# Optimization experiments

Hardware: AMD Instinct MI355X
Metric: run time of the kernel (lower is better)

The kernel has to match this reference:

```python
import jax, jax.numpy as jnp
import numpy as np

D_MODEL = 256
D_INNER = 512
D_STATE = 16
DT_RANK = 16
D_CONV = 4


def _layernorm(x, g, b):
    m = x.mean(-1, keepdims=True)
    v = jnp.mean((x - m) ** 2, axis=-1, keepdims=True)
    return (x - m) * jax.lax.rsqrt(v + 1e-5) * g + b


def _mamba(x, p):
    # x: (B, L, D); faithful to mamba_ssm Mamba forward (selective_scan_ref)
    in_w, conv_w, conv_b, xp_w, dt_w, dt_b, A_log, Dp, out_w = p
    B, L, _ = x.shape
    xz = x @ in_w.T                                   # (B, L, 2*d_inner)
    xi, z = jnp.split(xz, 2, axis=-1)
    # causal depthwise conv over time (d_conv=4), truncated to L
    xpad = jnp.pad(xi, ((0, 0), (D_CONV - 1, 0), (0, 0)))
    xc = conv_b + sum(xpad[:, k:k + L, :] * conv_w[:, k] for k in range(D_CONV))
    xc = jax.nn.silu(xc)                              # u: (B, L, d_inner)
    dbl = xc @ xp_w.T                                 # (B, L, dt_rank + 2*d_state)
    dt = dbl[..., :DT_RANK]
    Bm = dbl[..., DT_RANK:DT_RANK + D_STATE]          # (B, L, n)
    Cm = dbl[..., DT_RANK + D_STATE:]                 # (B, L, n)
    delta = jax.nn.softplus(dt @ dt_w.T + dt_b)       # (B, L, d_inner)
    A = -jnp.exp(A_log)                               # (d_inner, n)
    dA = jnp.exp(jnp.einsum('bld,dn->bldn', delta, A))
    dBu = jnp.einsum('bld,bln,bld->bldn', delta, Bm, xc)

    def step(h, inp):
        dA_t, dBu_t, C_t = inp
        h = dA_t * h + dBu_t                          # (B, d_inner, n)
        return h, jnp.einsum('bdn,bn->bd', h, C_t)

    h0 = jnp.zeros((B, D_INNER, D_STATE), x.dtype)
    _, ys = jax.lax.scan(step, h0, (dA.transpose(1, 0, 2, 3),
                                    dBu.transpose(1, 0, 2, 3),
                                    Cm.transpose(1, 0, 2)))
    y = ys.transpose(1, 0, 2) + xc * Dp               # (B, L, d_inner)
    y = y * jax.nn.silu(z)
    return y @ out_w.T                                # (B, L, D)


def _encoder(layer_params, x):
    # layer_params leaves have leading axis = num_layers (3)
    def step(carry, p):
        h = _layernorm(carry, p[0], p[1])
        return h + _mamba(h, p[2:]), None
    out, _ = jax.lax.scan(step, x, layer_params)
    return out


def _forward(x1, x2, x3, x4, audio, vis_w, vis_b, ln_g, ln_b, in_w, conv_w,
             conv_b, xp_w, dt_w, dt_b, A_log, Dp, out_w, gate_w, gate_b):
    gamma = 1.0
    bt = x1.shape[0]
    B = bt // 10
    d = x1.shape[1]
    pooled = [x.mean((2, 3)).reshape(B, 10, d) for x in (x1, x2, x3, x4)]
    vis = [p @ vis_w[i].T + vis_b[i] for i, p in enumerate(pooled)]
    # encoders 0..3: audio, 4..7: video scales
    stacked = jnp.stack([audio, audio, audio, audio] + vis)     # (8, B, 10, d)
    enc_params = (ln_g, ln_b, in_w, conv_w, conv_b, xp_w, dt_w, dt_b, A_log, Dp, out_w)
    outs = jax.vmap(_encoder)(enc_params, stacked)              # (8, B, 10, d)
    gates = jax.nn.silu(jnp.einsum('ebld,eod->eblo', outs, gate_w)
                        + gate_b[:, None, None, :])
    # NOTE: gate1 is reshaped WITHOUT transpose (faithful to original code)
    ag1 = gates[0].reshape(bt, d, 1, 1)
    ag2 = jnp.transpose(gates[1], (1, 0, 2)).reshape(bt, d, 1, 1)
    ag3 = jnp.transpose(gates[2], (1, 0, 2)).reshape(bt, d, 1, 1)
    ag4 = jnp.transpose(gates[3], (1, 0, 2)).reshape(bt, d, 1, 1)
    vg = sum(jnp.transpose(gates[4 + i], (1, 0, 2)).reshape(bt, d)
             for i in range(4)) / 4.0
    x1o = x1 + ag1 * x1 * gamma
    x2o = x2 + ag2 * x2 * gamma
    x3o = x3 + ag3 * x3 * gamma
    x4o = x4 + ag4 * x4 * gamma
    af = audio.reshape(bt, d)
    ao = (af + vg * af * gamma)[:, :, None]                     # (bt, d, 1)
    return (x4o, x3o, x2o, x1o, ao)


def setup_inputs() -> dict:
    key = jax.random.key(0)
    ks = jax.random.split(key, 24)
    s = 0.05
    n = lambda k, shp: jax.random.normal(k, shp, dtype=jnp.float32)
    inp = {
        'x1': n(ks[0], (40, 256, 56, 56)),
        'x2': n(ks[1], (40, 256, 28, 28)),
        'x3': n(ks[2], (40, 256, 14, 14)),
        'x4': n(ks[3], (40, 256, 7, 7)),
        'audio': n(ks[4], (4, 10, 256)),
        'vis_w': n(ks[5], (4, 256, 256)) * s,
        'vis_b': n(ks[6], (4, 256)) * s,
        'ln_g': jnp.ones((8, 3, 256), jnp.float32),
        'ln_b': jnp.zeros((8, 3, 256), jnp.float32),
        'in_w': n(ks[7], (8, 3, 1024, 256)) * s,
        'conv_w': n(ks[8], (8, 3, 512, 4)) * s,
        'conv_b': n(ks[9], (8, 3, 512)) * s,
        'xp_w': n(ks[10], (8, 3, 48, 512)) * s,
        'dt_w': n(ks[11], (8, 3, 512, 16)) * s,
        'dt_b': n(ks[12], (8, 3, 512)) * s,
        'A_log': jnp.broadcast_to(jnp.log(jnp.arange(1, 17, dtype=jnp.float32)),
                                  (8, 3, 512, 16)) + 0.0,
        'Dp': jnp.ones((8, 3, 512), jnp.float32),
        'out_w': n(ks[13], (8, 3, 256, 512)) * s,
        'gate_w': n(ks[14], (8, 256, 256)) * s,
        'gate_b': n(ks[15], (8, 256)) * s,
    }
    return inp


def reference(x1, x2, x3, x4, audio, vis_w, vis_b, ln_g, ln_b, in_w, conv_w,
              conv_b, xp_w, dt_w, dt_b, A_log, Dp, out_w, gate_w, gate_b):
    return _forward(x1, x2, x3, x4, audio, vis_w, vis_b, ln_g, ln_b, in_w,
                    conv_w, conv_b, xp_w, dt_w, dt_b, A_log, Dp, out_w,
                    gate_w, gate_b)
```

## Files before the change

kernel.cpp:

```cpp
#include <hip/hip_runtime.h>

#define DM 256
#define DI 512
#define NL 10

#define WS_POOLED 0
#define WS_SX     122880
#define WS_SH     204800
#define WS_XC     286720
#define WS_SZ     450560
#define WS_Y2     614400

__device__ __forceinline__ float dot4(float4 a, float4 b) {
    return a.x*b.x + a.y*b.y + a.z*b.z + a.w*b.w;
}
__device__ __forceinline__ float silu(float x) {
    return x / (1.f + __expf(-x));
}

__global__ void pool_kernel(const float* __restrict__ x1, const float* __restrict__ x2,
                            const float* __restrict__ x3, const float* __restrict__ x4,
                            const float* __restrict__ audio, float* __restrict__ ws)
{
    if (blockIdx.x >= 10240) {
        const int idx = blockIdx.x - 10240, e = idx >> 2, b = idx & 3;
        float* sx = ws + WS_SX + (e*4+b)*2560;
        for (int i = threadIdx.x; i < 2560; i += 256) sx[i] = audio[b*2560 + i];
        return;
    }
    float* pooled = ws + WS_POOLED;
    int wid  = (blockIdx.x * blockDim.x + threadIdx.x) >> 6;
    int lane = threadIdx.x & 63;
    int img = wid / 10240;
    int r   = wid % 10240;
    const float* src; int hw;
    if      (img == 0) { src = x1; hw = 3136; }
    else if (img == 1) { src = x2; hw = 784; }
    else if (img == 2) { src = x3; hw = 196; }
    else               { src = x4; hw = 49; }
    const float* row = src + (size_t)r * hw;
    float s = 0.f;
    if (hw == 49) {
        if (lane < 49) s = row[lane];
    } else {
        int n4 = hw >> 2;
        for (int j = lane; j < n4; j += 64) {
            float4 v = *(const float4*)(row + j*4);
            s += v.x + v.y + v.z + v.w;
        }
    }
    #pragma unroll
    for (int off = 32; off; off >>= 1) s += __shfl_down(s, off);
    if (lane == 0) pooled[img*10240 + r] = s / (float)hw;
}

__global__ __launch_bounds__(256)
void build_kernel(const float* __restrict__ vis_w, const float* __restrict__ vis_b,
                  float* __restrict__ ws)
{
    __shared__ float act[NL*DM];
    const int tid = threadIdx.x, bi = blockIdx.x;
    const int img = bi >> 6, b = (bi >> 4) & 3, tile = bi & 15;
    const float* pooled = ws + WS_POOLED + img*10240 + b*2560;
    for (int i = tid; i < 640; i += 256)
        ((float4*)act)[i] = ((const float4*)pooled)[i];
    __syncthreads();
    const int wave = tid >> 6, lane = tid & 63;
    const int c4 = lane >> 4, k16 = lane & 15;
    const int col = tile*16 + wave*4 + c4;
    const float* wp = vis_w + img*65536 + col*256 + k16*4;
    float acc[NL];
    #pragma unroll
    for (int l = 0; l < NL; l++) acc[l] = 0.f;
    #pragma unroll
    for (int ko = 0; ko < 4; ko++) {
        float4 wv = *(const float4*)(wp + ko*64);
        #pragma unroll
        for (int l = 0; l < NL; l++)
            acc[l] += dot4(wv, *(const float4*)(&act[l*256 + ko*64 + k16*4]));
    }
    #pragma unroll
    for (int l = 0; l < NL; l++) {
        acc[l] += __shfl_xor(acc[l], 1);
        acc[l] += __shfl_xor(acc[l], 2);
        acc[l] += __shfl_xor(acc[l], 4);
        acc[l] += __shfl_xor(acc[l], 8);
    }
    if (k16 == 0) {
        float bias = vis_b[img*256 + col];
        float* sx = ws + WS_SX + ((img+4)*4+b)*2560;
        #pragma unroll
        for (int l = 0; l < NL; l++) sx[l*256 + col] = bias + acc[l];
    }
}

__global__ __launch_bounds__(256)
void lnxz_kernel(const float* __restrict__ ln_g, const float* __restrict__ ln_b,
                 const float* __restrict__ in_w, const float* __restrict__ conv_w,
                 const float* __restrict__ conv_b, float* __restrict__ ws, int layer)
{
    __shared__ float act[NL*DM];
    const int tid = threadIdx.x, bi = blockIdx.x;
    const int e = bi >> 8, b = (bi >> 6) & 3, tile = bi & 63;
    const int el = e*3 + layer;
    const int wave = tid >> 6, lane = tid & 63;
    const float* sx = ws + WS_SX + (e*4+b)*2560;
    float* shg = ws + WS_SH + (e*4+b)*2560;

    for (int l = wave; l < NL; l += 4) {
        float4 v = *(const float4*)(sx + l*256 + lane*4);
        float s = v.x+v.y+v.z+v.w, ss = dot4(v, v);
        #pragma unroll
        for (int off = 32; off; off >>= 1) { s += __shfl_xor(s, off); ss += __shfl_xor(ss, off); }
        float m = s * (1.f/256.f);
        float rs = rsqrtf(ss*(1.f/256.f) - m*m + 1e-5f);
        float4 gv = *(const float4*)(ln_g + el*256 + lane*4);
        float4 bv = *(const float4*)(ln_b + el*256 + lane*4);
        float4 hv;
        hv.x = (v.x-m)*rs*gv.x + bv.x;
        hv.y = (v.y-m)*rs*gv.y + bv.y;
        hv.z = (v.z-m)*rs*gv.z + bv.z;
        hv.w = (v.w-m)*rs*gv.w + bv.w;
        *(float4*)(&act[l*256 + lane*4]) = hv;
        if (tile == 0) *(float4*)(shg + l*256 + lane*4) = hv;
    }
    __syncthreads();

    const int c4 = lane >> 4, k16 = lane & 15;
    const int col = tile*16 + wave*4 + c4;
    const float* wp = in_w + (size_t)el*262144 + (size_t)col*256 + k16*4;
    float acc[NL];
    #pragma unroll
    for (int l = 0; l < NL; l++) acc[l] = 0.f;
    #pragma unroll
    for (int ko = 0; ko < 4; ko++) {
        float4 wv = *(const float4*)(wp + ko*64);
        #pragma unroll
        for (int l = 0; l < NL; l++)
            acc[l] += dot4(wv, *(const float4*)(&act[l*256 + ko*64 + k16*4]));
    }
    #pragma unroll
    for (int l = 0; l < NL; l++) {
        acc[l] += __shfl_xor(acc[l], 1);
        acc[l] += __shfl_xor(acc[l], 2);
        acc[l] += __shfl_xor(acc[l], 4);
        acc[l] += __shfl_xor(acc[l], 8);
    }
    if (k16 == 0) {
        if (col < 512) {
            float4 cw = *(const float4*)(conv_w + el*2048 + col*4);
            float cb = conv_b[el*512 + col];
            float* xc = ws + WS_XC + (e*4+b)*5120;
            float x0 = 0.f, x1 = 0.f, x2 = 0.f;
            #pragma unroll
            for (int l = 0; l < NL; l++) {
                float x3 = acc[l];
                float a = cb + x3*cw.w + x2*cw.z + x1*cw.y + x0*cw.x;
                xc[l*512 + col] = silu(a);
                x0 = x1; x1 = x2; x2 = x3;
            }
        } else {
            float* sz = ws + WS_SZ + (e*4+b)*5120;
            const int d = col - 512;
            #pragma unroll
            for (int l = 0; l < NL; l++) sz[l*512 + d] = silu(acc[l]);
        }
    }
}

__global__ __launch_bounds__(256)
void dso2_kernel(const float* __restrict__ xp_w, const float* __restrict__ dt_w,
                 const float* __restrict__ dt_b, const float* __restrict__ A_log,
                 const float* __restrict__ Dp,   float* __restrict__ ws, int layer)
{
    __shared__ float xc_l[NL*DI];
    __shared__ float dbl_l[NL*48];
    const int tid = threadIdx.x, bi = blockIdx.x;
    const int eb = bi >> 3, slice = bi & 7;
    const int e = eb >> 2;
    const int el = e*3 + layer;
    const float* xc = ws + WS_XC + eb*5120;

    for (int i = tid; i < 1280; i += 256)
        ((float4*)xc_l)[i] = ((const float4*)xc)[i];
    __syncthreads();

    {
        const int wave = tid >> 6, lane = tid & 63;
        const int c4 = lane >> 4, k16 = lane & 15;
        for (int i = 0; i < 30; i++) {
            int t = wave*120 + i*4 + c4;
            int l = t / 48, r = t % 48;
            const float* wp = xp_w + el*24576 + r*512 + k16*4;
            float p = 0.f;
            #pragma unroll
            for (int ko = 0; ko < 8; ko++)
                p += dot4(*(const float4*)(wp + ko*64),
                          *(const float4*)(&xc_l[l*512 + ko*64 + k16*4]));
            p += __shfl_xor(p, 1);
            p += __shfl_xor(p, 2);
            p += __shfl_xor(p, 4);
            p += __shfl_xor(p, 8);
            if (k16 == 0) dbl_l[l*48 + r] = p;
        }
    }
    __syncthreads();

    {
        const int d = slice*64 + (tid >> 2);
        const int q = tid & 3;
        const float* dwp = dt_w + el*8192 + d*16;
        float4 dw0 = *(const float4*)(dwp);
        float4 dw1 = *(const float4*)(dwp + 4);
        float4 dw2 = *(const float4*)(dwp + 8);
        float4 dw3 = *(const float4*)(dwp + 12);
        float dbv = dt_b[el*512 + d];
        float Dpv = Dp[el*512 + d];
        float Av[4];
        #pragma unroll
        for (int j = 0; j < 4; j++)
            Av[j] = -__expf(A_log[el*8192 + d*16 + q*4 + j]);
        const float* sz = ws + WS_SZ + eb*5120;
        float* y2 = ws + WS_Y2 + eb*5120;
        float h[4];
        #pragma unroll
        for (int j = 0; j < 4; j++) h[j] = 0.f;
        #pragma unroll
        for (int l = 0; l < NL; l++) {
            float4 t0 = *(const float4*)(&dbl_l[l*48]);
            float4 t1 = *(const float4*)(&dbl_l[l*48 + 4]);
            float4 t2 = *(const float4*)(&dbl_l[l*48 + 8]);
            float4 t3 = *(const float4*)(&dbl_l[l*48 + 12]);
            float a = dbv + dot4(t0,dw0) + dot4(t1,dw1) + dot4(t2,dw2) + dot4(t3,dw3);
            float dl = fmaxf(a, 0.f) + log1pf(__expf(-fabsf(a)));
            float xcv = xc_l[l*512 + d];
            float du = dl * xcv;
            float y = 0.f;
            #pragma unroll
            for (int j = 0; j < 4; j++) {
                float Bn = dbl_l[l*48 + 16 + q*4 + j];
                float Cn = dbl_l[l*48 + 32 + q*4 + j];
                h[j] = __expf(dl*Av[j])*h[j] + du*Bn;
                y += h[j]*Cn;
            }
            y += __shfl_xor(y, 1);
            y += __shfl_xor(y, 2);
            if (q == 0) y2[l*512 + d] = (y + xcv*Dpv) * sz[l*512 + d];
        }
    }
}

__global__ __launch_bounds__(256)
void out_kernel(const float* __restrict__ out_w, float* __restrict__ ws, int layer)
{
    __shared__ float act[NL*DI];
    const int tid = threadIdx.x, bi = blockIdx.x;
    const int e = bi >> 6, b = (bi >> 4) & 3, tile = bi & 15;
    const int el = e*3 + layer;
    const float* y2 = ws + WS_Y2 + (e*4+b)*5120;
    for (int i = tid; i < 1280; i += 256)
        ((float4*)act)[i] = ((const float4*)y2)[i];
    __syncthreads();

    const int wave = tid >> 6, lane = tid & 63;
    const int c4 = lane >> 4, k16 = lane & 15;
    const int col = tile*16 + wave*4 + c4;
    const float* wp = out_w + (size_t)el*131072 + (size_t)col*512 + k16*4;
    float acc[NL];
    #pragma unroll
    for (int l = 0; l < NL; l++) acc[l] = 0.f;
    #pragma unroll
    for (int ko = 0; ko < 8; ko++) {
        float4 wv = *(const float4*)(wp + ko*64);
        #pragma unroll
        for (int l = 0; l < NL; l++)
            acc[l] += dot4(wv, *(const float4*)(&act[l*512 + ko*64 + k16*4]));
    }
    #pragma unroll
    for (int l = 0; l < NL; l++) {
        acc[l] += __shfl_xor(acc[l], 1);
        acc[l] += __shfl_xor(acc[l], 2);
        acc[l] += __shfl_xor(acc[l], 4);
        acc[l] += __shfl_xor(acc[l], 8);
    }
    if (k16 == 0) {
        const float* sh = ws + WS_SH + (e*4+b)*2560;
        float* sx = ws + WS_SX + (e*4+b)*2560;
        #pragma unroll
        for (int l = 0; l < NL; l++) sx[l*256 + col] = sh[l*256 + col] + acc[l];
    }
}

__global__ void scale_ao_gate_kernel(const float* __restrict__ x1, const float* __restrict__ x2,
                                     const float* __restrict__ x3, const float* __restrict__ x4,
                                     const float* __restrict__ audio,
                                     const float* __restrict__ gate_w,
                                     const float* __restrict__ gate_b,
                                     const float* __restrict__ ws, float* __restrict__ out)
{
    int wid  = (blockIdx.x * blockDim.x + threadIdx.x) >> 6;
    int lane = threadIdx.x & 63;
    const float* sxB = ws + WS_SX;
    if (wid >= 51200) return;
    if (wid >= 40960) {
        int i = wid - 40960;
        int bt = i >> 8, c = i & 255;
        int b = bt & 3, l = bt >> 2;
        int c4 = lane >> 4, k16 = lane & 15;
        int e = 4 + c4;
        const float* gw = gate_w + e*65536 + c*256;
        const float* sxrow = sxB + (e*4+b)*2560 + l*256;
        float p = 0.f;
        #pragma unroll
        for (int ko = 0; ko < 4; ko++)
            p += dot4(*(const float4*)(gw + ko*64 + k16*4),
                      *(const float4*)(sxrow + ko*64 + k16*4));
        p += __shfl_xor(p, 1);
        p += __shfl_xor(p, 2);
        p += __shfl_xor(p, 4);
        p += __shfl_xor(p, 8);
        float g = silu(gate_b[e*256 + c] + p);
        g += __shfl_xor(g, 16);
        g += __shfl_xor(g, 32);
        if (lane == 0) out[42649600 + i] = audio[bt*256 + c] * (1.f + 0.25f*g);
        return;
    }
    int t = wid / 10240, r = wid % 10240;
    int bt = r >> 8, c = r & 255;
    int e, b, l;
    if (t == 3) { e = 0; b = bt / 10; l = bt % 10; }
    else        { e = 3 - t; b = bt & 3; l = bt >> 2; }
    const float* gw = gate_w + e*65536 + c*256;
    const float* sxrow = sxB + (e*4+b)*2560 + l*256;
    float p = dot4(*(const float4*)(gw + lane*4), *(const float4*)(sxrow + lane*4));
    #pragma unroll
    for (int off = 32; off; off >>= 1) p += __shfl_xor(p, off);
    float scale = 1.f + silu(gate_b[e*256 + c] + p);

    const float* src; int hw; size_t obase;
    if      (t == 0) { src = x4; hw = 49;   obase = 0; }
    else if (t == 1) { src = x3; hw = 196;  obase = 501760; }
    else if (t == 2) { src = x2; hw = 784;  obase = 2508800; }
    else             { src = x1; hw = 3136; obase = 10536960; }
    const float* row = src + (size_t)r * hw;
    float* orow = out + obase + (size_t)r * hw;
    if (hw == 49) {
        if (lane < 49) orow[lane] = row[lane] * scale;
    } else {
        int n4 = hw >> 2;
        for (int j = lane; j < n4; j += 64) {
            float4 v = *(const float4*)(row + j*4);
            v.x *= scale; v.y *= scale; v.z *= scale; v.w *= scale;
            *(float4*)(orow + j*4) = v;
        }
    }
}

extern "C" void kernel_launch(void* const* d_in, const int* in_sizes, int n_in,
                              void* d_out, int out_size, void* d_ws, size_t ws_size,
                              hipStream_t stream)
{
    const float* x1     = (const float*)d_in[0];
    const float* x2     = (const float*)d_in[1];
    const float* x3     = (const float*)d_in[2];
    const float* x4     = (const float*)d_in[3];
    const float* audio  = (const float*)d_in[4];
    const float* vis_w  = (const float*)d_in[5];
    const float* vis_b  = (const float*)d_in[6];
    const float* ln_g   = (const float*)d_in[7];
    const float* ln_b   = (const float*)d_in[8];
    const float* in_w   = (const float*)d_in[9];
    const float* conv_w = (const float*)d_in[10];
    const float* conv_b = (const float*)d_in[11];
    const float* xp_w   = (const float*)d_in[12];
    const float* dt_w   = (const float*)d_in[13];
    const float* dt_b   = (const float*)d_in[14];
    const float* A_log  = (const float*)d_in[15];
    const float* Dp     = (const float*)d_in[16];
    const float* out_w  = (const float*)d_in[17];
    const float* gate_w = (const float*)d_in[18];
    const float* gate_b = (const float*)d_in[19];

    float* ws  = (float*)d_ws;
    float* out = (float*)d_out;

    pool_kernel<<<dim3(10256), dim3(256), 0, stream>>>(x1, x2, x3, x4, audio, ws);
    build_kernel<<<dim3(256), dim3(256), 0, stream>>>(vis_w, vis_b, ws);
    for (int layer = 0; layer < 3; layer++) {
        lnxz_kernel<<<dim3(2048), dim3(256), 0, stream>>>(ln_g, ln_b, in_w, conv_w,
                                                          conv_b, ws, layer);
        dso2_kernel<<<dim3(256), dim3(256), 0, stream>>>(xp_w, dt_w, dt_b, A_log,
                                                         Dp, ws, layer);
        out_kernel<<<dim3(512), dim3(256), 0, stream>>>(out_w, ws, layer);
    }
    scale_ao_gate_kernel<<<dim3(12800), dim3(256), 0, stream>>>(x1, x2, x3, x4, audio,
                                                                gate_w, gate_b, ws, out);
}
```

Before: 260.4 us.

## Split x_proj and selective scan into separate kernels to remove redundant projection

The fused kernel had each of 8 slices per (expert,batch) recompute the full 48-wide x_proj for all timesteps. The projection now runs in a separate kernel where each of the 8 blocks computes only 6 of the 48 outputs and writes them to a new workspace region. A second kernel does the scan with one thread per channel holding all 16 states, so the shuffle reduction goes away. This removes the 8x redundant projection work but adds an extra launch, a global round trip for dbl, and the scan kernel now runs only 128 small blocks with more registers per thread.

```diff
diff --git a/kernel.cpp b/kernel.cpp
--- a/kernel.cpp
+++ b/kernel.cpp
@@ -10,6 +10,7 @@
 #define WS_XC     286720
 #define WS_SZ     450560
 #define WS_Y2     614400
+#define WS_DBL    778240
 
 __device__ __forceinline__ float dot4(float4 a, float4 b) {
     return a.x*b.x + a.y*b.y + a.z*b.z + a.w*b.w;
@@ -169,28 +170,25 @@
 }
 
 __global__ __launch_bounds__(256)
-void dso2_kernel(const float* __restrict__ xp_w, const float* __restrict__ dt_w,
-                 const float* __restrict__ dt_b, const float* __restrict__ A_log,
-                 const float* __restrict__ Dp,   float* __restrict__ ws, int layer)
+void dbl_kernel(const float* __restrict__ xp_w, float* __restrict__ ws, int layer)
 {
     __shared__ float xc_l[NL*DI];
-    __shared__ float dbl_l[NL*48];
     const int tid = threadIdx.x, bi = blockIdx.x;
-    const int eb = bi >> 3, slice = bi & 7;
-    const int e = eb >> 2;
+    const int e = bi >> 5, b = (bi >> 3) & 3, s = bi & 7;
     const int el = e*3 + layer;
-    const float* xc = ws + WS_XC + eb*5120;
-
+    const float* xc = ws + WS_XC + (e*4+b)*5120;
     for (int i = tid; i < 1280; i += 256)
         ((float4*)xc_l)[i] = ((const float4*)xc)[i];
     __syncthreads();
 
-    {
-        const int wave = tid >> 6, lane = tid & 63;
-        const int c4 = lane >> 4, k16 = lane & 15;
-        for (int i = 0; i < 30; i++) {
-            int t = wave*120 + i*4 + c4;
-            int l = t / 48, r = t % 48;
+    const int wave = tid >> 6, lane = tid & 63;
+    const int c4 = lane >> 4, k16 = lane & 15;
+    float* dbl = ws + WS_DBL + (e*4+b)*480;
+    #pragma unroll
+    for (int i = 0; i < 4; i++) {
+        int t = wave*16 + i*4 + c4;
+        if (t < 60) {
+            int l = t / 6, r = s*6 + t % 6;
             const float* wp = xp_w + el*24576 + r*512 + k16*4;
             float p = 0.f;
             #pragma unroll
@@ -201,52 +199,60 @@
             p += __shfl_xor(p, 2);
             p += __shfl_xor(p, 4);
             p += __shfl_xor(p, 8);
-            if (k16 == 0) dbl_l[l*48 + r] = p;
+            if (k16 == 0) dbl[l*48 + r] = p;
         }
     }
+}
+
+__global__ __launch_bounds__(128)
+void scan_kernel(const float* __restrict__ dt_w, const float* __restrict__ dt_b,
+                 const float* __restrict__ A_log, const float* __restrict__ Dp,
+                 float* __restrict__ ws, int layer)
+{
+    __shared__ float dbl_l[NL*48];
+    const int tid = threadIdx.x, bi = blockIdx.x;
+    const int e = bi >> 4, b = (bi >> 2) & 3, ch = bi & 3;
+    const int el = e*3 + layer;
+    const int eb = e*4 + b;
+    for (int i = tid; i < 480; i += 128) dbl_l[i] = ws[WS_DBL + eb*480 + i];
     __syncthreads();
 
-    {
-        const int d = slice*64 + (tid >> 2);
-        const int q = tid & 3;
-        const float* dwp = dt_w + el*8192 + d*16;
-        float4 dw0 = *(const float4*)(dwp);
-        float4 dw1 = *(const float4*)(dwp + 4);
-        float4 dw2 = *(const float4*)(dwp + 8);
-        float4 dw3 = *(const float4*)(dwp + 12);
-        float dbv = dt_b[el*512 + d];
-        float Dpv = Dp[el*512 + d];
-        float Av[4];
-        #pragma unroll
-        for (int j = 0; j < 4; j++)
-            Av[j] = -__expf(A_log[el*8192 + d*16 + q*4 + j]);
-        const float* sz = ws + WS_SZ + eb*5120;
-        float* y2 = ws + WS_Y2 + eb*5120;
-        float h[4];
-        #pragma unroll
-        for (int j = 0; j < 4; j++) h[j] = 0.f;
-        #pragma unroll
-        for (int l = 0; l < NL; l++) {
-            float4 t0 = *(const float4*)(&dbl_l[l*48]);
-            float4 t1 = *(const float4*)(&dbl_l[l*48 + 4]);
-            float4 t2 = *(const float4*)(&dbl_l[l*48 + 8]);
-            float4 t3 = *(const float4*)(&dbl_l[l*48 + 12]);
-            float a = dbv + dot4(t0,dw0) + dot4(t1,dw1) + dot4(t2,dw2) + dot4(t3,dw3);
-            float dl = fmaxf(a, 0.f) + log1pf(__expf(-fabsf(a)));
-            float xcv = xc_l[l*512 + d];
-            float du = dl * xcv;
-            float y = 0.f;
-            #pragma unroll
-            for (int j = 0; j < 4; j++) {
-                float Bn = dbl_l[l*48 + 16 + q*4 + j];
-                float Cn = dbl_l[l*48 + 32 + q*4 + j];
-                h[j] = __expf(dl*Av[j])*h[j] + du*Bn;
-                y += h[j]*Cn;
-            }
-            y += __shfl_xor(y, 1);
-            y += __shfl_xor(y, 2);
-            if (q == 0) y2[l*512 + d] = (y + xcv*Dpv) * sz[l*512 + d];
+    const int d = ch*128 + tid;
+    const float* dwp = dt_w + el*8192 + d*16;
+    float4 dw0 = *(const float4*)(dwp);
+    float4 dw1 = *(const float4*)(dwp + 4);
+    float4 dw2 = *(const float4*)(dwp + 8);
+    float4 dw3 = *(const float4*)(dwp + 12);
+    float dbv = dt_b[el*512 + d];
+    float Dpv = Dp[el*512 + d];
+    float Av[16];
+    #pragma unroll
+    for (int n = 0; n < 16; n++) Av[n] = -__expf(A_log[el*8192 + d*16 + n]);
+    const float* xc = ws + WS_XC + eb*5120;
+    const float* sz = ws + WS_SZ + eb*5120;
+    float* y2 = ws + WS_Y2 + eb*5120;
+    float h[16];
+    #pragma unroll
+    for (int n = 0; n < 16; n++) h[n] = 0.f;
+    #pragma unroll
+    for (int l = 0; l < NL; l++) {
+        float4 t0 = *(const float4*)(&dbl_l[l*48]);
+        float4 t1 = *(const float4*)(&dbl_l[l*48 + 4]);
+        float4 t2 = *(const float4*)(&dbl_l[l*48 + 8]);
+        float4 t3 = *(const float4*)(&dbl_l[l*48 + 12]);
+        float a = dbv + dot4(t0,dw0) + dot4(t1,dw1) + dot4(t2,dw2) + dot4(t3,dw3);
+        float dl = fmaxf(a, 0.f) + log1pf(__expf(-fabsf(a)));
+        float xcv = xc[l*512 + d];
+        float du = dl * xcv;
+        float y = 0.f;
+        #pragma unroll
+        for (int n = 0; n < 16; n++) {
+            float Bn = dbl_l[l*48 + 16 + n];
+            float Cn = dbl_l[l*48 + 32 + n];
+            h[n] = __expf(dl*Av[n])*h[n] + du*Bn;
+            y += h[n]*Cn;
         }
+        y2[l*512 + d] = (y + xcv*Dpv) * sz[l*512 + d];
     }
 }
 
@@ -389,8 +395,8 @@
     for (int layer = 0; layer < 3; layer++) {
         lnxz_kernel<<<dim3(2048), dim3(256), 0, stream>>>(ln_g, ln_b, in_w, conv_w,
                                                           conv_b, ws, layer);
-        dso2_kernel<<<dim3(256), dim3(256), 0, stream>>>(xp_w, dt_w, dt_b, A_log,
-                                                         Dp, ws, layer);
+        dbl_kernel<<<dim3(256), dim3(256), 0, stream>>>(xp_w, ws, layer);
+        scan_kernel<<<dim3(128), dim3(128), 0, stream>>>(dt_w, dt_b, A_log, Dp, ws, layer);
         out_kernel<<<dim3(512), dim3(256), 0, stream>>>(out_w, ws, layer);
     }
     scale_ao_gate_kernel<<<dim3(12800), dim3(256), 0, stream>>>(x1, x2, x3, x4, audio,
```

Result: faster. 229.2 us (-12.0%).
